# Kernel tuning notes

Measured on AMD Instinct MI355X. Metric: run time of the kernel, lower is better.

## Reference

```python
import jax, jax.numpy as jnp
import numpy as np

BS, SEQ = 8, 2048
IN_F, OUT_F = 2048, 2048
N_SPLITS, N_SKILLS, RANK = 4, 8, 16
LORA_ALPHA = 32
SCALING = LORA_ALPHA / RANK


def setup_inputs() -> dict:
    key = jax.random.key(0)
    k1, k2, k3, k4 = jax.random.split(key, 4)
    inp = jax.random.normal(k1, (BS, SEQ, IN_F), dtype=jnp.float32)
    weights = jax.random.uniform(k2, (BS, N_SPLITS, N_SKILLS), dtype=jnp.float32)
    # kaiming-uniform-like init scale for lora_a; lora_b nonzero for a meaningful baseline
    std = (2.0 / (1.0 + 5.0)) ** 0.5 / (IN_F ** 0.5)
    lora_a = jax.random.uniform(k3, (N_SPLITS, N_SKILLS, IN_F // N_SPLITS, RANK),
                                dtype=jnp.float32, minval=-std, maxval=std)
    lora_b = jax.random.normal(k4, (N_SPLITS, N_SKILLS, RANK, OUT_F // N_SPLITS),
                               dtype=jnp.float32) * 0.02
    return {"input": inp, "weights": weights, "lora_a": lora_a, "lora_b": lora_b}


def reference(input, weights, lora_a, lora_b):
    bs = weights.shape[0]
    # mix per-skill LoRA factors: b=batch, q=split, s=skill, d=feat, r=rank
    A = jnp.einsum('bqs,qsdr->bqdr', weights, lora_a)          # [bs, q, in/q, r]
    B = jnp.einsum('bqs,qsrd->bqrd', weights, lora_b)          # [bs, q, r, out/q]
    A = A.reshape(bs, IN_F, RANK)                              # [bs, in, r]
    B = jnp.transpose(B, (0, 2, 1, 3)).reshape(bs, RANK, OUT_F)  # [bs, r, out]
    # batched low-rank matmul: [bs, seq, in] @ [bs, in, r] @ [bs, r, out]
    adapter_out = jnp.einsum('bsr,bro->bso', jnp.einsum('bsi,bir->bsr', input, A), B)
    return adapter_out * SCALING
```

## Files before the change

### kernel.cpp

```cpp
#include <hip/hip_runtime.h>
#include <hip/hip_bf16.h>
#include <cstdint>
#include <cstddef>

#define RANK 16

typedef __attribute__((ext_vector_type(8))) short bf16x8;
typedef __attribute__((ext_vector_type(4))) float f32x4;

static __device__ __forceinline__ short f2bf(float f) {
  __hip_bfloat16 h = __float2bfloat16(f);
  return *reinterpret_cast<short*>(&h);
}

__global__ __launch_bounds__(256) void skilled_lora_mix(
    const float* __restrict__ w,
    const float* __restrict__ la,
    const float* __restrict__ lb,
    __hip_bfloat16* __restrict__ Amt,
    float* __restrict__ Bm)
{
  const int j = blockIdx.x * 256 + threadIdx.x;
  if (j < 65536) {
    const int r0 = (j & 3) * 4;
    const int k  = (j >> 2) & 2047;
    const int b  = j >> 13;
    const int q  = k >> 9;
    const int d  = k & 511;
    const float* wb = w + (b * 4 + q) * 8;
    float4 acc = make_float4(0.f, 0.f, 0.f, 0.f);
#pragma unroll
    for (int s = 0; s < 8; ++s) {
      const float ws = wb[s];
      const float4 v = *reinterpret_cast<const float4*>(
          la + (size_t)(((q * 8 + s) * 512 + d) * 16 + r0));
      acc.x = fmaf(ws, v.x, acc.x);
      acc.y = fmaf(ws, v.y, acc.y);
      acc.z = fmaf(ws, v.z, acc.z);
      acc.w = fmaf(ws, v.w, acc.w);
    }
    Amt[((size_t)(b * 16 + r0 + 0)) * 2048 + k] = __float2bfloat16(acc.x);
    Amt[((size_t)(b * 16 + r0 + 1)) * 2048 + k] = __float2bfloat16(acc.y);
    Amt[((size_t)(b * 16 + r0 + 2)) * 2048 + k] = __float2bfloat16(acc.z);
    Amt[((size_t)(b * 16 + r0 + 3)) * 2048 + k] = __float2bfloat16(acc.w);
  } else {
    const int jj = j - 65536;
    const int o  = (jj & 511) * 4;
    const int r  = (jj >> 9) & 15;
    const int b  = jj >> 13;
    const int q  = o >> 9;
    const int dd = o & 511;
    const float* wb = w + (b * 4 + q) * 8;
    float4 acc = make_float4(0.f, 0.f, 0.f, 0.f);
#pragma unroll
    for (int s = 0; s < 8; ++s) {
      const float ws = wb[s];
      const float4 v = *reinterpret_cast<const float4*>(
          lb + (size_t)(((q * 8 + s) * 16 + r) * 512 + dd));
      acc.x = fmaf(ws, v.x, acc.x);
      acc.y = fmaf(ws, v.y, acc.y);
      acc.z = fmaf(ws, v.z, acc.z);
      acc.w = fmaf(ws, v.w, acc.w);
    }
    acc.x *= 2.f; acc.y *= 2.f; acc.z *= 2.f; acc.w *= 2.f;
    *reinterpret_cast<float4*>(Bm + (size_t)((b * 16 + r) * 2048 + o)) = acc;
  }
}

__global__ __launch_bounds__(256, 8) void lora_phase_a(
    const float* __restrict__ X,
    const __hip_bfloat16* __restrict__ Amt,
    float* __restrict__ tmp_p)
{
  __shared__ float lds[4 * 16 * 68];

  const int tid  = threadIdx.x;
  const int lane = tid & 63;
  const int wv   = tid >> 6;
  const int b    = blockIdx.x >> 8;
  const int tile = (blockIdx.x >> 1) & 127;
  const int ks   = blockIdx.x & 1;
  const int row0 = tile * 16;
  const int k0   = ks * 1024 + wv * 256;
  const int m    = lane & 15;
  const int g    = lane >> 4;

  float* stage = lds + wv * (16 * 68);

  const int ms = lane >> 2;
  const int cs = (lane & 3) * 4;

  const float* Xb = X + ((size_t)(b * 2048 + row0)) * 2048 + k0;
  const __hip_bfloat16* Ap = Amt + ((size_t)(b * 16 + m)) * 2048 + k0 + g * 8;

  f32x4 acc = {0.f, 0.f, 0.f, 0.f};

  for (int c = 0; c < 4; ++c) {
    const int kc = c * 64;
#pragma unroll
    for (int i = 0; i < 4; ++i) {
      const float4 v = *reinterpret_cast<const float4*>(
          Xb + (size_t)ms * 2048 + kc + i * 16 + cs);
      *reinterpret_cast<float4*>(&stage[ms * 68 + i * 16 + cs]) = v;
    }
#pragma unroll
    for (int h = 0; h < 2; ++h) {
      const float4 xlo = *reinterpret_cast<const float4*>(
          &stage[m * 68 + h * 32 + g * 8]);
      const float4 xhi = *reinterpret_cast<const float4*>(
          &stage[m * 68 + h * 32 + g * 8 + 4]);
      bf16x8 afrag;
      afrag[0] = f2bf(xlo.x); afrag[1] = f2bf(xlo.y);
      afrag[2] = f2bf(xlo.z); afrag[3] = f2bf(xlo.w);
      afrag[4] = f2bf(xhi.x); afrag[5] = f2bf(xhi.y);
      afrag[6] = f2bf(xhi.z); afrag[7] = f2bf(xhi.w);
      const bf16x8 bfrag = *reinterpret_cast<const bf16x8*>(
          Ap + (size_t)(c * 2 + h) * 32);
      acc = __builtin_amdgcn_mfma_f32_16x16x32_bf16(afrag, bfrag, acc, 0, 0, 0);
    }
  }

  __syncthreads();
  float* part = lds;
#pragma unroll
  for (int v = 0; v < 4; ++v)
    part[(wv * 16 + g * 4 + v) * 17 + m] = acc[v];
  __syncthreads();

  const int row = tid >> 4;
  const int r   = tid & 15;
  const float s = part[(0 * 16 + row) * 17 + r] + part[(1 * 16 + row) * 17 + r]
                + part[(2 * 16 + row) * 17 + r] + part[(3 * 16 + row) * 17 + r];
  tmp_p[((size_t)((ks * 8 + b) * 2048 + row0 + row)) * RANK + r] = s;
}

__global__ __launch_bounds__(256, 2) void lora_phase_b(
    const float* __restrict__ tmp_p,
    const float* __restrict__ Bm,
    float* __restrict__ out)
{
  const int tid  = threadIdx.x;
  const int b    = blockIdx.x >> 8;
  const int rt   = (blockIdx.x >> 2) & 63;
  const int og   = blockIdx.x & 3;
  const int row0 = rt * 32;
  const int o0   = og * 512 + tid * 2;

  const float* Bb = Bm + (size_t)b * (RANK * 2048) + o0;
  float2 B2[RANK];
#pragma unroll
  for (int r = 0; r < RANK; ++r)
    B2[r] = *reinterpret_cast<const float2*>(Bb + (size_t)r * 2048);

  const float* tp0 = tmp_p + ((size_t)(b * 2048 + row0)) * RANK;
  const float* tp1 = tmp_p + ((size_t)((8 + b) * 2048 + row0)) * RANK;
  float* op = out + ((size_t)(b * 2048 + row0)) * 2048 + o0;

#pragma unroll 4
  for (int rr = 0; rr < 32; ++rr) {
    const float4 u0 = *reinterpret_cast<const float4*>(tp0 + rr * RANK);
    const float4 u1 = *reinterpret_cast<const float4*>(tp0 + rr * RANK + 4);
    const float4 u2 = *reinterpret_cast<const float4*>(tp0 + rr * RANK + 8);
    const float4 u3 = *reinterpret_cast<const float4*>(tp0 + rr * RANK + 12);
    const float4 v0 = *reinterpret_cast<const float4*>(tp1 + rr * RANK);
    const float4 v1 = *reinterpret_cast<const float4*>(tp1 + rr * RANK + 4);
    const float4 v2 = *reinterpret_cast<const float4*>(tp1 + rr * RANK + 8);
    const float4 v3 = *reinterpret_cast<const float4*>(tp1 + rr * RANK + 12);
    const float t0x = u0.x + v0.x, t0y = u0.y + v0.y, t0z = u0.z + v0.z, t0w = u0.w + v0.w;
    const float t1x = u1.x + v1.x, t1y = u1.y + v1.y, t1z = u1.z + v1.z, t1w = u1.w + v1.w;
    const float t2x = u2.x + v2.x, t2y = u2.y + v2.y, t2z = u2.z + v2.z, t2w = u2.w + v2.w;
    const float t3x = u3.x + v3.x, t3y = u3.y + v3.y, t3z = u3.z + v3.z, t3w = u3.w + v3.w;
    float2 a = make_float2(0.f, 0.f);
    a.x = fmaf(t0x, B2[0].x,  a.x);  a.y = fmaf(t0x, B2[0].y,  a.y);
    a.x = fmaf(t0y, B2[1].x,  a.x);  a.y = fmaf(t0y, B2[1].y,  a.y);
    a.x = fmaf(t0z, B2[2].x,  a.x);  a.y = fmaf(t0z, B2[2].y,  a.y);
    a.x = fmaf(t0w, B2[3].x,  a.x);  a.y = fmaf(t0w, B2[3].y,  a.y);
    a.x = fmaf(t1x, B2[4].x,  a.x);  a.y = fmaf(t1x, B2[4].y,  a.y);
    a.x = fmaf(t1y, B2[5].x,  a.x);  a.y = fmaf(t1y, B2[5].y,  a.y);
    a.x = fmaf(t1z, B2[6].x,  a.x);  a.y = fmaf(t1z, B2[6].y,  a.y);
    a.x = fmaf(t1w, B2[7].x,  a.x);  a.y = fmaf(t1w, B2[7].y,  a.y);
    a.x = fmaf(t2x, B2[8].x,  a.x);  a.y = fmaf(t2x, B2[8].y,  a.y);
    a.x = fmaf(t2y, B2[9].x,  a.x);  a.y = fmaf(t2y, B2[9].y,  a.y);
    a.x = fmaf(t2z, B2[10].x, a.x);  a.y = fmaf(t2z, B2[10].y, a.y);
    a.x = fmaf(t2w, B2[11].x, a.x);  a.y = fmaf(t2w, B2[11].y, a.y);
    a.x = fmaf(t3x, B2[12].x, a.x);  a.y = fmaf(t3x, B2[12].y, a.y);
    a.x = fmaf(t3y, B2[13].x, a.x);  a.y = fmaf(t3y, B2[13].y, a.y);
    a.x = fmaf(t3z, B2[14].x, a.x);  a.y = fmaf(t3z, B2[14].y, a.y);
    a.x = fmaf(t3w, B2[15].x, a.x);  a.y = fmaf(t3w, B2[15].y, a.y);
    *reinterpret_cast<float2*>(op + (size_t)rr * 2048) = a;
  }
}

extern "C" void kernel_launch(void* const* d_in, const int* in_sizes, int n_in,
                              void* d_out, int out_size, void* d_ws, size_t ws_size,
                              hipStream_t stream) {
  const float* input = (const float*)d_in[0];
  const float* w     = (const float*)d_in[1];
  const float* la    = (const float*)d_in[2];
  const float* lb    = (const float*)d_in[3];
  float* outp = (float*)d_out;

  __hip_bfloat16* Amt = (__hip_bfloat16*)d_ws;
  float* Bm    = (float*)((char*)d_ws + (size_t)8 * 16 * 2048 * 2);
  float* tmp_p = Bm + 8 * RANK * 2048;

  skilled_lora_mix<<<512, 256, 0, stream>>>(w, la, lb, Amt, Bm);
  lora_phase_a<<<2048, 256, 0, stream>>>(input, Amt, tmp_p);
  lora_phase_b<<<2048, 256, 0, stream>>>(tmp_p, Bm, outp);
}
```

Measured before the change: 65.94 us.

## Merge phase A and B into one kernel and software-pipeline across batch chunks

Combines the X·A reduction and the T·B expansion into one kernel whose blocks branch on block index. It launches five staggered grids, each running phase A for the next two batches alongside phase B for the previous two. The aim is to overlap the read-heavy X pass with the write-heavy output pass so HBM read and write traffic run at the same time. In exchange it adds launches, and the merged kernel now uses launch bounds of 2 for the phase A path, which may lower its occupancy.

After: 98.33 us. +49.1%, slower.

```diff
diff --git a/kernel.cpp b/kernel.cpp
--- a/kernel.cpp
+++ b/kernel.cpp
@@ -67,127 +67,128 @@
   }
 }
 
-__global__ __launch_bounds__(256, 8) void lora_phase_a(
+__global__ __launch_bounds__(256, 2) void lora_pipe(
     const float* __restrict__ X,
     const __hip_bfloat16* __restrict__ Amt,
-    float* __restrict__ tmp_p)
+    const float* __restrict__ Bm,
+    float* __restrict__ tmp_p,
+    float* __restrict__ out,
+    int aBase, int nA, int bBase, int nB)
 {
   __shared__ float lds[4 * 16 * 68];
 
-  const int tid  = threadIdx.x;
-  const int lane = tid & 63;
-  const int wv   = tid >> 6;
-  const int b    = blockIdx.x >> 8;
-  const int tile = (blockIdx.x >> 1) & 127;
-  const int ks   = blockIdx.x & 1;
-  const int row0 = tile * 16;
-  const int k0   = ks * 1024 + wv * 256;
-  const int m    = lane & 15;
-  const int g    = lane >> 4;
-
-  float* stage = lds + wv * (16 * 68);
-
-  const int ms = lane >> 2;
-  const int cs = (lane & 3) * 4;
-
-  const float* Xb = X + ((size_t)(b * 2048 + row0)) * 2048 + k0;
-  const __hip_bfloat16* Ap = Amt + ((size_t)(b * 16 + m)) * 2048 + k0 + g * 8;
-
-  f32x4 acc = {0.f, 0.f, 0.f, 0.f};
-
-  for (int c = 0; c < 4; ++c) {
-    const int kc = c * 64;
-#pragma unroll
-    for (int i = 0; i < 4; ++i) {
-      const float4 v = *reinterpret_cast<const float4*>(
-          Xb + (size_t)ms * 2048 + kc + i * 16 + cs);
-      *reinterpret_cast<float4*>(&stage[ms * 68 + i * 16 + cs]) = v;
-    }
-#pragma unroll
-    for (int h = 0; h < 2; ++h) {
-      const float4 xlo = *reinterpret_cast<const float4*>(
-          &stage[m * 68 + h * 32 + g * 8]);
-      const float4 xhi = *reinterpret_cast<const float4*>(
-          &stage[m * 68 + h * 32 + g * 8 + 4]);
-      bf16x8 afrag;
-      afrag[0] = f2bf(xlo.x); afrag[1] = f2bf(xlo.y);
-      afrag[2] = f2bf(xlo.z); afrag[3] = f2bf(xlo.w);
-      afrag[4] = f2bf(xhi.x); afrag[5] = f2bf(xhi.y);
-      afrag[6] = f2bf(xhi.z); afrag[7] = f2bf(xhi.w);
-      const bf16x8 bfrag = *reinterpret_cast<const bf16x8*>(
-          Ap + (size_t)(c * 2 + h) * 32);
-      acc = __builtin_amdgcn_mfma_f32_16x16x32_bf16(afrag, bfrag, acc, 0, 0, 0);
-    }
-  }
-
-  __syncthreads();
-  float* part = lds;
-#pragma unroll
-  for (int v = 0; v < 4; ++v)
-    part[(wv * 16 + g * 4 + v) * 17 + m] = acc[v];
-  __syncthreads();
-
-  const int row = tid >> 4;
-  const int r   = tid & 15;
-  const float s = part[(0 * 16 + row) * 17 + r] + part[(1 * 16 + row) * 17 + r]
-                + part[(2 * 16 + row) * 17 + r] + part[(3 * 16 + row) * 17 + r];
-  tmp_p[((size_t)((ks * 8 + b) * 2048 + row0 + row)) * RANK + r] = s;
-}
-
-__global__ __launch_bounds__(256, 2) void lora_phase_b(
-    const float* __restrict__ tmp_p,
-    const float* __restrict__ Bm,
-    float* __restrict__ out)
-{
-  const int tid  = threadIdx.x;
-  const int b    = blockIdx.x >> 8;
-  const int rt   = (blockIdx.x >> 2) & 63;
-  const int og   = blockIdx.x & 3;
-  const int row0 = rt * 32;
-  const int o0   = og * 512 + tid * 2;
-
-  const float* Bb = Bm + (size_t)b * (RANK * 2048) + o0;
-  float2 B2[RANK];
-#pragma unroll
-  for (int r = 0; r < RANK; ++r)
-    B2[r] = *reinterpret_cast<const float2*>(Bb + (size_t)r * 2048);
-
-  const float* tp0 = tmp_p + ((size_t)(b * 2048 + row0)) * RANK;
-  const float* tp1 = tmp_p + ((size_t)((8 + b) * 2048 + row0)) * RANK;
-  float* op = out + ((size_t)(b * 2048 + row0)) * 2048 + o0;
+  const int tid = threadIdx.x;
+
+  if ((int)blockIdx.x < nA * 256) {
+    const int u    = blockIdx.x;
+    const int lane = tid & 63;
+    const int wv   = tid >> 6;
+    const int b    = aBase + (u >> 8);
+    const int tile = (u >> 1) & 127;
+    const int ks   = u & 1;
+    const int row0 = tile * 16;
+    const int k0   = ks * 1024 + wv * 256;
+    const int m    = lane & 15;
+    const int g    = lane >> 4;
+
+    float* stage = lds + wv * (16 * 68);
+    const int ms = lane >> 2;
+    const int cs = (lane & 3) * 4;
+
+    const float* Xb = X + ((size_t)(b * 2048 + row0)) * 2048 + k0;
+    const __hip_bfloat16* Ap = Amt + ((size_t)(b * 16 + m)) * 2048 + k0 + g * 8;
+
+    f32x4 acc = {0.f, 0.f, 0.f, 0.f};
+
+    for (int c = 0; c < 4; ++c) {
+      const int kc = c * 64;
+#pragma unroll
+      for (int i = 0; i < 4; ++i) {
+        const float4 v = *reinterpret_cast<const float4*>(
+            Xb + (size_t)ms * 2048 + kc + i * 16 + cs);
+        *reinterpret_cast<float4*>(&stage[ms * 68 + i * 16 + cs]) = v;
+      }
+#pragma unroll
+      for (int h = 0; h < 2; ++h) {
+        const float4 xlo = *reinterpret_cast<const float4*>(
+            &stage[m * 68 + h * 32 + g * 8]);
+        const float4 xhi = *reinterpret_cast<const float4*>(
+            &stage[m * 68 + h * 32 + g * 8 + 4]);
+        bf16x8 afrag;
+        afrag[0] = f2bf(xlo.x); afrag[1] = f2bf(xlo.y);
+        afrag[2] = f2bf(xlo.z); afrag[3] = f2bf(xlo.w);
+        afrag[4] = f2bf(xhi.x); afrag[5] = f2bf(xhi.y);
+        afrag[6] = f2bf(xhi.z); afrag[7] = f2bf(xhi.w);
+        const bf16x8 bfrag = *reinterpret_cast<const bf16x8*>(
+            Ap + (size_t)(c * 2 + h) * 32);
+        acc = __builtin_amdgcn_mfma_f32_16x16x32_bf16(afrag, bfrag, acc, 0, 0, 0);
+      }
+    }
+
+    __syncthreads();
+    float* part = lds;
+#pragma unroll
+    for (int v = 0; v < 4; ++v)
+      part[(wv * 16 + g * 4 + v) * 17 + m] = acc[v];
+    __syncthreads();
+
+    const int row = tid >> 4;
+    const int r   = tid & 15;
+    const float s = part[(0 * 16 + row) * 17 + r] + part[(1 * 16 + row) * 17 + r]
+                  + part[(2 * 16 + row) * 17 + r] + part[(3 * 16 + row) * 17 + r];
+    tmp_p[((size_t)((ks * 8 + b) * 2048 + row0 + row)) * RANK + r] = s;
+
+  } else {
+    const int u    = blockIdx.x - nA * 256;
+    const int b    = bBase + (u >> 8);
+    const int rt   = (u >> 2) & 63;
+    const int og   = u & 3;
+    const int row0 = rt * 32;
+    const int o0   = og * 512 + tid * 2;
+
+    const float* Bb = Bm + (size_t)b * (RANK * 2048) + o0;
+    float2 B2[RANK];
+#pragma unroll
+    for (int r = 0; r < RANK; ++r)
+      B2[r] = *reinterpret_cast<const float2*>(Bb + (size_t)r * 2048);
+
+    const float* tp0 = tmp_p + ((size_t)(b * 2048 + row0)) * RANK;
+    const float* tp1 = tmp_p + ((size_t)((8 + b) * 2048 + row0)) * RANK;
+    float* op = out + ((size_t)(b * 2048 + row0)) * 2048 + o0;
 
 #pragma unroll 4
-  for (int rr = 0; rr < 32; ++rr) {
-    const float4 u0 = *reinterpret_cast<const float4*>(tp0 + rr * RANK);
-    const float4 u1 = *reinterpret_cast<const float4*>(tp0 + rr * RANK + 4);
-    const float4 u2 = *reinterpret_cast<const float4*>(tp0 + rr * RANK + 8);
-    const float4 u3 = *reinterpret_cast<const float4*>(tp0 + rr * RANK + 12);
-    const float4 v0 = *reinterpret_cast<const float4*>(tp1 + rr * RANK);
-    const float4 v1 = *reinterpret_cast<const float4*>(tp1 + rr * RANK + 4);
-    const float4 v2 = *reinterpret_cast<const float4*>(tp1 + rr * RANK + 8);
-    const float4 v3 = *reinterpret_cast<const float4*>(tp1 + rr * RANK + 12);
-    const float t0x = u0.x + v0.x, t0y = u0.y + v0.y, t0z = u0.z + v0.z, t0w = u0.w + v0.w;
-    const float t1x = u1.x + v1.x, t1y = u1.y + v1.y, t1z = u1.z + v1.z, t1w = u1.w + v1.w;
-    const float t2x = u2.x + v2.x, t2y = u2.y + v2.y, t2z = u2.z + v2.z, t2w = u2.w + v2.w;
-    const float t3x = u3.x + v3.x, t3y = u3.y + v3.y, t3z = u3.z + v3.z, t3w = u3.w + v3.w;
-    float2 a = make_float2(0.f, 0.f);
-    a.x = fmaf(t0x, B2[0].x,  a.x);  a.y = fmaf(t0x, B2[0].y,  a.y);
-    a.x = fmaf(t0y, B2[1].x,  a.x);  a.y = fmaf(t0y, B2[1].y,  a.y);
-    a.x = fmaf(t0z, B2[2].x,  a.x);  a.y = fmaf(t0z, B2[2].y,  a.y);
-    a.x = fmaf(t0w, B2[3].x,  a.x);  a.y = fmaf(t0w, B2[3].y,  a.y);
-    a.x = fmaf(t1x, B2[4].x,  a.x);  a.y = fmaf(t1x, B2[4].y,  a.y);
-    a.x = fmaf(t1y, B2[5].x,  a.x);  a.y = fmaf(t1y, B2[5].y,  a.y);
-    a.x = fmaf(t1z, B2[6].x,  a.x);  a.y = fmaf(t1z, B2[6].y,  a.y);
-    a.x = fmaf(t1w, B2[7].x,  a.x);  a.y = fmaf(t1w, B2[7].y,  a.y);
-    a.x = fmaf(t2x, B2[8].x,  a.x);  a.y = fmaf(t2x, B2[8].y,  a.y);
-    a.x = fmaf(t2y, B2[9].x,  a.x);  a.y = fmaf(t2y, B2[9].y,  a.y);
-    a.x = fmaf(t2z, B2[10].x, a.x);  a.y = fmaf(t2z, B2[10].y, a.y);
-    a.x = fmaf(t2w, B2[11].x, a.x);  a.y = fmaf(t2w, B2[11].y, a.y);
-    a.x = fmaf(t3x, B2[12].x, a.x);  a.y = fmaf(t3x, B2[12].y, a.y);
-    a.x = fmaf(t3y, B2[13].x, a.x);  a.y = fmaf(t3y, B2[13].y, a.y);
-    a.x = fmaf(t3z, B2[14].x, a.x);  a.y = fmaf(t3z, B2[14].y, a.y);
-    a.x = fmaf(t3w, B2[15].x, a.x);  a.y = fmaf(t3w, B2[15].y, a.y);
-    *reinterpret_cast<float2*>(op + (size_t)rr * 2048) = a;
+    for (int rr = 0; rr < 32; ++rr) {
+      const float4 u0 = *reinterpret_cast<const float4*>(tp0 + rr * RANK);
+      const float4 u1 = *reinterpret_cast<const float4*>(tp0 + rr * RANK + 4);
+      const float4 u2 = *reinterpret_cast<const float4*>(tp0 + rr * RANK + 8);
+      const float4 u3 = *reinterpret_cast<const float4*>(tp0 + rr * RANK + 12);
+      const float4 v0 = *reinterpret_cast<const float4*>(tp1 + rr * RANK);
+      const float4 v1 = *reinterpret_cast<const float4*>(tp1 + rr * RANK + 4);
+      const float4 v2 = *reinterpret_cast<const float4*>(tp1 + rr * RANK + 8);
+      const float4 v3 = *reinterpret_cast<const float4*>(tp1 + rr * RANK + 12);
+      const float t0x = u0.x + v0.x, t0y = u0.y + v0.y, t0z = u0.z + v0.z, t0w = u0.w + v0.w;
+      const float t1x = u1.x + v1.x, t1y = u1.y + v1.y, t1z = u1.z + v1.z, t1w = u1.w + v1.w;
+      const float t2x = u2.x + v2.x, t2y = u2.y + v2.y, t2z = u2.z + v2.z, t2w = u2.w + v2.w;
+      const float t3x = u3.x + v3.x, t3y = u3.y + v3.y, t3z = u3.z + v3.z, t3w = u3.w + v3.w;
+      float2 a = make_float2(0.f, 0.f);
+      a.x = fmaf(t0x, B2[0].x,  a.x);  a.y = fmaf(t0x, B2[0].y,  a.y);
+      a.x = fmaf(t0y, B2[1].x,  a.x);  a.y = fmaf(t0y, B2[1].y,  a.y);
+      a.x = fmaf(t0z, B2[2].x,  a.x);  a.y = fmaf(t0z, B2[2].y,  a.y);
+      a.x = fmaf(t0w, B2[3].x,  a.x);  a.y = fmaf(t0w, B2[3].y,  a.y);
+      a.x = fmaf(t1x, B2[4].x,  a.x);  a.y = fmaf(t1x, B2[4].y,  a.y);
+      a.x = fmaf(t1y, B2[5].x,  a.x);  a.y = fmaf(t1y, B2[5].y,  a.y);
+      a.x = fmaf(t1z, B2[6].x,  a.x);  a.y = fmaf(t1z, B2[6].y,  a.y);
+      a.x = fmaf(t1w, B2[7].x,  a.x);  a.y = fmaf(t1w, B2[7].y,  a.y);
+      a.x = fmaf(t2x, B2[8].x,  a.x);  a.y = fmaf(t2x, B2[8].y,  a.y);
+      a.x = fmaf(t2y, B2[9].x,  a.x);  a.y = fmaf(t2y, B2[9].y,  a.y);
+      a.x = fmaf(t2z, B2[10].x, a.x);  a.y = fmaf(t2z, B2[10].y, a.y);
+      a.x = fmaf(t2w, B2[11].x, a.x);  a.y = fmaf(t2w, B2[11].y, a.y);
+      a.x = fmaf(t3x, B2[12].x, a.x);  a.y = fmaf(t3x, B2[12].y, a.y);
+      a.x = fmaf(t3y, B2[13].x, a.x);  a.y = fmaf(t3y, B2[13].y, a.y);
+      a.x = fmaf(t3z, B2[14].x, a.x);  a.y = fmaf(t3z, B2[14].y, a.y);
+      a.x = fmaf(t3w, B2[15].x, a.x);  a.y = fmaf(t3w, B2[15].y, a.y);
+      *reinterpret_cast<float2*>(op + (size_t)rr * 2048) = a;
+    }
   }
 }
 
@@ -205,6 +206,10 @@
   float* tmp_p = Bm + 8 * RANK * 2048;
 
   skilled_lora_mix<<<512, 256, 0, stream>>>(w, la, lb, Amt, Bm);
-  lora_phase_a<<<2048, 256, 0, stream>>>(input, Amt, tmp_p);
-  lora_phase_b<<<2048, 256, 0, stream>>>(tmp_p, Bm, outp);
-}
+
+  lora_pipe<<< 512, 256, 0, stream>>>(input, Amt, Bm, tmp_p, outp, 0, 2, 0, 0);
+  lora_pipe<<<1024, 256, 0, stream>>>(input, Amt, Bm, tmp_p, outp, 2, 2, 0, 2);
+  lora_pipe<<<1024, 256, 0, stream>>>(input, Amt, Bm, tmp_p, outp, 4, 2, 2, 2);
+  lora_pipe<<<1024, 256, 0, stream>>>(input, Amt, Bm, tmp_p, outp, 6, 2, 4, 2);
+  lora_pipe<<< 512, 256, 0, stream>>>(input, Amt, Bm, tmp_p, outp, 0, 0, 6, 2);
+}
```
